# Kernel optimization log

Measured on AMD Instinct MI355X. Metric: run time of the kernel, lower is better.

Reference implementation:

```python
import jax, jax.numpy as jnp
import numpy as np

V = 12000; WE = 1000; FEAT = 2048; FE = 1024; H = 1024; AH = 512; NREG = 36; B = 128; T = 17
PAD_ID = 0


def _lstm_cell(x, h, c, wih, whh, bih, bhh):
    # torch LSTMCell: gates ordered (input, forget, cell, output)
    g = x @ wih.T + h @ whh.T + bih + bhh
    i, f, gg, o = jnp.split(g, 4, axis=-1)
    c_new = jax.nn.sigmoid(f) * c + jax.nn.sigmoid(i) * jnp.tanh(gg)
    h_new = jax.nn.sigmoid(o) * jnp.tanh(c_new)
    return h_new, c_new


def setup_inputs() -> dict:
    key = jax.random.key(0)
    ks = jax.random.split(key, 24)
    s = 0.02
    emb_w = jax.random.normal(ks[0], (V, WE), jnp.float32) * s
    emb_w = emb_w.at[PAD_ID].set(0.0)  # padding_idx row is zero
    inp = {
        'fc_feats': jax.random.normal(ks[1], (B, FEAT), jnp.float32),
        'att_feats': jax.random.normal(ks[2], (B, NREG, FEAT), jnp.float32),
        'captions': jax.random.randint(ks[3], (B, T), 0, V, jnp.int64),
        'emb_w': emb_w,
        'fc_w': jax.random.normal(ks[4], (FEAT, FE), jnp.float32) * s,
        'fc_b': jnp.zeros((FE,), jnp.float32),
        'atte_w': jax.random.normal(ks[5], (FEAT, FE), jnp.float32) * s,
        'atte_b': jnp.zeros((FE,), jnp.float32),
        'ctx_w': jax.random.normal(ks[6], (FE, AH), jnp.float32) * s,
        'ctx_b': jnp.zeros((AH,), jnp.float32),
        'attl_wih': jax.random.normal(ks[7], (4 * H, H + FE + WE), jnp.float32) * s,
        'attl_whh': jax.random.normal(ks[8], (4 * H, H), jnp.float32) * s,
        'attl_bih': jnp.zeros((4 * H,), jnp.float32),
        'attl_bhh': jnp.zeros((4 * H,), jnp.float32),
        'h2att_w': jax.random.normal(ks[9], (H, AH), jnp.float32) * s,
        'h2att_b': jnp.zeros((AH,), jnp.float32),
        'alpha_w': jax.random.normal(ks[10], (AH,), jnp.float32) * s,
        'alpha_b': jnp.zeros((), jnp.float32),
        'langl_wih': jax.random.normal(ks[11], (4 * H, FE + H), jnp.float32) * s,
        'langl_whh': jax.random.normal(ks[12], (4 * H, H), jnp.float32) * s,
        'langl_bih': jnp.zeros((4 * H,), jnp.float32),
        'langl_bhh': jnp.zeros((4 * H,), jnp.float32),
        'cls_w': jax.random.normal(ks[13], (H, V), jnp.float32) * s,
        'cls_b': jnp.zeros((V,), jnp.float32),
    }
    return inp


def _forward(fc_feats, att_feats, captions, emb_w, fc_w, fc_b, atte_w, atte_b,
             ctx_w, ctx_b, attl_wih, attl_whh, attl_bih, attl_bhh,
             h2att_w, h2att_b, alpha_w, alpha_b,
             langl_wih, langl_whh, langl_bih, langl_bhh, cls_w, cls_b):
    # _prepare_features (eval mode: dropout is identity)
    fc_e = jax.nn.relu(fc_feats @ fc_w + fc_b)                 # [B, FE]
    att_e = jax.nn.relu(att_feats @ atte_w + atte_b)           # [B, N, FE]
    p_att = att_e @ ctx_w + ctx_b                              # [B, N, AH]
    bsz = fc_feats.shape[0]
    h0 = jnp.zeros((bsz, H), fc_feats.dtype)

    def step(carry, it):
        h_att, c_att, h_lang, c_lang = carry
        w = jax.nn.relu(emb_w[it])                             # [B, WE]
        x_att = jnp.concatenate([h_lang, fc_e, w], axis=1)
        h_att, c_att = _lstm_cell(x_att, h_att, c_att, attl_wih, attl_whh, attl_bih, attl_bhh)
        # Attention
        hq = h_att @ h2att_w + h2att_b                          # [B, AH]
        e = jnp.tanh(p_att + hq[:, None, :]) @ alpha_w + alpha_b  # [B, N]
        alpha = jax.nn.softmax(e, axis=1)
        att_res = jnp.einsum('bn,bnd->bd', alpha, att_e)        # [B, FE]
        x_lang = jnp.concatenate([att_res, h_att], axis=1)
        h_lang, c_lang = _lstm_cell(x_lang, h_lang, c_lang, langl_wih, langl_whh, langl_bih, langl_bhh)
        logprobs = jax.nn.log_softmax(h_lang @ cls_w + cls_b, axis=1)  # [B, V]
        return (h_att, c_att, h_lang, c_lang), logprobs

    its = captions[:, :-1].T  # [T-1, B]
    _, outs = jax.lax.scan(step, (h0, h0, h0, h0), its)
    return jnp.transpose(outs, (1, 0, 2))  # [B, T-1, V]


def reference(fc_feats, att_feats, captions, emb_w, fc_w, fc_b, atte_w, atte_b,
              ctx_w, ctx_b, attl_wih, attl_whh, attl_bih, attl_bhh,
              h2att_w, h2att_b, alpha_w, alpha_b,
              langl_wih, langl_whh, langl_bih, langl_bhh, cls_w, cls_b):
    return _forward(fc_feats, att_feats, captions, emb_w, fc_w, fc_b, atte_w, atte_b,
                    ctx_w, ctx_b, attl_wih, attl_whh, attl_bih, attl_bhh,
                    h2att_w, h2att_b, alpha_w, alpha_b,
                    langl_wih, langl_whh, langl_bih, langl_bhh, cls_w, cls_b)
```

## Files before the change

kernel.cpp:

```cpp
#include <hip/hip_runtime.h>
#include <cstddef>
#include <cstdint>

constexpr int CV    = 12000;
constexpr int CVP2  = 12288;
constexpr int CWE   = 1000;
constexpr int CFEAT = 2048;
constexpr int CFE   = 1024;
constexpr int CH    = 1024;
constexpr int CAH   = 512;
constexpr int CNREG = 36;
constexpr int CB    = 128;
constexpr int CT    = 17;
constexpr int G4    = 4096;
constexpr int XH    = 2048;
constexpr int XL3   = 3072;

#define CDIV(a,b) (((a)+(b)-1)/(b))

typedef __bf16 bf16_t;
typedef __bf16 bf16x8 __attribute__((ext_vector_type(8)));
typedef __bf16 bf16x4 __attribute__((ext_vector_type(4)));
typedef float  f32x4  __attribute__((ext_vector_type(4)));

typedef __attribute__((address_space(3))) uint32_t lds_u32;
typedef const __attribute__((address_space(1))) uint32_t glb_u32;

struct Seg { const bf16_t* A; const bf16_t* W; int lda, ldw, kt; };

template<bool RELU, bool OUTBF, int SWZ>
__global__ __launch_bounds__(256)
void pre_gemm(Seg s0, int inner, const float* __restrict__ bias1,
              void* __restrict__ Cout, int ldc)
{
    const int tid = threadIdx.x;
    const int wid = tid >> 6, lane = tid & 63;
    const int wr = wid >> 1, wc = wid & 1;
    const int llo = lane & 15, lhi = lane >> 4;
    const int nb = gridDim.x, id = blockIdx.x;
    const int sw = (id & 7) * (nb >> 3) + (id >> 3);
    int m0, n0;
    if (SWZ == 1)      { n0 = (sw / inner) * 64;  m0 = (sw % inner) * 128; }
    else if (SWZ == 2) { m0 = (sw / inner) * 128; n0 = (sw % inner) * 64;  }
    else {
        const int xcd = id & 7, idx = id >> 3;
        m0 = (((xcd >> 2) << 3) + (idx & 7)) * 128;
        n0 = (((xcd & 3) << 4) + (idx >> 3)) * 64;
    }

    __shared__ __align__(16) uint8_t sm[2][24576];

    const int TT = s0.kt;
    f32x4 acc[4][2] = {};
    uint4 ra[4], rb[2];
    const int srow = tid >> 3, sc = tid & 7;
    const int cswz = (sc ^ (srow & 7)) << 4;

    auto load_tile = [&](int ti) {
        const int k0 = ti << 6;
        #pragma unroll
        for (int i = 0; i < 4; ++i)
            ra[i] = *(const uint4*)(s0.A + (size_t)(m0 + i * 32 + srow) * s0.lda + k0 + sc * 8);
        #pragma unroll
        for (int i = 0; i < 2; ++i)
            rb[i] = *(const uint4*)(s0.W + (size_t)(n0 + i * 32 + srow) * s0.ldw + k0 + sc * 8);
    };
    auto write_tile = [&](int buf) {
        uint8_t* base = sm[buf];
        #pragma unroll
        for (int i = 0; i < 4; ++i) *(uint4*)(base + (i * 32 + srow) * 128 + cswz) = ra[i];
        #pragma unroll
        for (int i = 0; i < 2; ++i) *(uint4*)(base + 16384 + (i * 32 + srow) * 128 + cswz) = rb[i];
    };
    auto compute = [&](int buf) {
        const uint8_t* base = sm[buf];
        const int r7 = llo & 7;
        #pragma unroll
        for (int kk = 0; kk < 2; ++kk) {
            const int coff = ((kk * 4 + lhi) ^ r7) << 4;
            bf16x8 af[4], bg[2];
            #pragma unroll
            for (int fm = 0; fm < 4; ++fm)
                af[fm] = *(const bf16x8*)(base + (wr * 64 + fm * 16 + llo) * 128 + coff);
            #pragma unroll
            for (int fn = 0; fn < 2; ++fn)
                bg[fn] = *(const bf16x8*)(base + 16384 + (wc * 32 + fn * 16 + llo) * 128 + coff);
            #pragma unroll
            for (int fm = 0; fm < 4; ++fm)
                #pragma unroll
                for (int fn = 0; fn < 2; ++fn)
                    acc[fm][fn] = __builtin_amdgcn_mfma_f32_16x16x32_bf16(
                        af[fm], bg[fn], acc[fm][fn], 0, 0, 0);
        }
    };

    load_tile(0); write_tile(0);
    load_tile(1);
    __syncthreads();
    int cur = 0;
    for (int ti = 0; ti < TT; ++ti) {
        if (ti + 1 < TT) write_tile(cur ^ 1);
        if (ti + 2 < TT) load_tile(ti + 2);
        compute(cur);
        __syncthreads();
        cur ^= 1;
    }

    if (OUTBF) {
        bf16_t* st = (bf16_t*)sm[0];
        #pragma unroll
        for (int fn = 0; fn < 2; ++fn) {
            const int lcol = wc * 32 + fn * 16 + llo;
            const float b = bias1 ? bias1[n0 + lcol] : 0.f;
            #pragma unroll
            for (int fm = 0; fm < 4; ++fm)
                #pragma unroll
                for (int r = 0; r < 4; ++r) {
                    float v = acc[fm][fn][r] + b;
                    if (RELU) v = fmaxf(v, 0.f);
                    st[(wr * 64 + fm * 16 + lhi * 4 + r) * 64 + lcol] = (bf16_t)v;
                }
        }
        __syncthreads();
        #pragma unroll
        for (int i = 0; i < 4; ++i) {
            const int q = tid + i * 256;
            const int row = q >> 3, ch = q & 7;
            *(uint4*)((bf16_t*)Cout + (size_t)(m0 + row) * ldc + n0 + ch * 8)
                = *(const uint4*)&st[row * 64 + ch * 8];
        }
    } else {
        const int colb = n0 + wc * 32;
        const int rowb = m0 + wr * 64 + lhi * 4;
        #pragma unroll
        for (int fn = 0; fn < 2; ++fn) {
            const int col = colb + fn * 16 + llo;
            const float b = bias1 ? bias1[col] : 0.f;
            #pragma unroll
            for (int fm = 0; fm < 4; ++fm)
                #pragma unroll
                for (int r = 0; r < 4; ++r) {
                    float v = acc[fm][fn][r] + b;
                    if (RELU) v = fmaxf(v, 0.f);
                    ((float*)Cout)[(size_t)(rowb + fm * 16 + r) * ldc + col] = v;
                }
        }
    }
}

__global__ __launch_bounds__(256)
void cls_gemm(const bf16_t* __restrict__ A, const bf16_t* __restrict__ W,
              const float* __restrict__ bias, bf16_t* __restrict__ Cout)
{
    const int tid = threadIdx.x;
    const int wid = tid >> 6, lane = tid & 63;
    const int wr = wid >> 1, wc = wid & 1;
    const int llo = lane & 15, lhi = lane >> 4;
    const int id = blockIdx.x;
    const int xcd = id & 7, idx = id >> 3;
    const int mg = xcd & 1, ng = xcd >> 1;
    const int m0 = (mg * 8 + (idx & 7)) * 128;
    const int n0 = (ng * 24 + (idx >> 3)) * 128;

    __shared__ __align__(16) uint8_t pool[65536];
    auto bufA = [&](int b) { return pool + b * 16384; };
    auto bufB = [&](int b) { return pool + 32768 + b * 16384; };

    constexpr int TT = 16;
    f32x4 acc[4][4] = {};
    uint4 ra[4], rbv[4];

    auto load_tile = [&](int ti) {
        const int k0 = ti << 6;
        #pragma unroll
        for (int i = 0; i < 4; ++i) {
            const int q = tid + i * 256;
            const int row = q >> 3, c = q & 7;
            ra[i]  = *(const uint4*)(A + (size_t)(m0 + row) * CH + k0 + c * 8);
            rbv[i] = *(const uint4*)(W + (size_t)(n0 + row) * CH + k0 + c * 8);
        }
    };
    auto write_tile = [&](int buf) {
        #pragma unroll
        for (int i = 0; i < 4; ++i) {
            const int q = tid + i * 256;
            const int row = q >> 3, c = q & 7;
            const int o = row * 128 + ((c ^ (row & 7)) << 4);
            *(uint4*)(bufA(buf) + o) = ra[i];
            *(uint4*)(bufB(buf) + o) = rbv[i];
        }
    };
    auto compute = [&](int buf) {
        const int r7 = llo & 7;
        #pragma unroll
        for (int kk = 0; kk < 2; ++kk) {
            const int coff = ((kk * 4 + lhi) ^ r7) << 4;
            bf16x8 af[4], bg[4];
            #pragma unroll
            for (int fm = 0; fm < 4; ++fm)
                af[fm] = *(const bf16x8*)(bufA(buf) + (wr * 64 + fm * 16 + llo) * 128 + coff);
            #pragma unroll
            for (int fn = 0; fn < 4; ++fn)
                bg[fn] = *(const bf16x8*)(bufB(buf) + (wc * 64 + fn * 16 + llo) * 128 + coff);
            #pragma unroll
            for (int fm = 0; fm < 4; ++fm)
                #pragma unroll
                for (int fn = 0; fn < 4; ++fn)
                    acc[fm][fn] = __builtin_amdgcn_mfma_f32_16x16x32_bf16(
                        af[fm], bg[fn], acc[fm][fn], 0, 0, 0);
        }
    };

    load_tile(0); write_tile(0);
    load_tile(1);
    __syncthreads();
    int cur = 0;
    for (int ti = 0; ti < TT; ++ti) {
        if (ti + 1 < TT) write_tile(cur ^ 1);
        if (ti + 2 < TT) load_tile(ti + 2);
        compute(cur);
        __syncthreads();
        cur ^= 1;
    }

    constexpr int STR = 136;
    bf16_t* st = (bf16_t*)pool;
    #pragma unroll
    for (int fn = 0; fn < 4; ++fn) {
        const int lcol = wc * 64 + fn * 16 + llo;
        const int col = n0 + lcol;
        const float b = (col < CV) ? bias[col] : 0.f;
        #pragma unroll
        for (int fm = 0; fm < 4; ++fm)
            #pragma unroll
            for (int r = 0; r < 4; ++r)
                st[(wr * 64 + fm * 16 + lhi * 4 + r) * STR + lcol]
                    = (bf16_t)(acc[fm][fn][r] + b);
    }
    __syncthreads();
    #pragma unroll
    for (int i = 0; i < 8; ++i) {
        const int q = tid + i * 256;
        const int row = q >> 4, ch = q & 15;
        *(uint4*)(Cout + (size_t)(m0 + row) * CVP2 + n0 + ch * 8)
            = *(const uint4*)&st[row * STR + ch * 8];
    }
}

template<int TAG>
__global__ __launch_bounds__(256)
void gate_split(const bf16_t* __restrict__ A, int lda,
                const bf16_t* __restrict__ W, int ldw, int ktz,
                bf16_t* __restrict__ gpart)
{
    const int tid = threadIdx.x;
    const int w = tid >> 6, lane = tid & 63;
    const int llo = lane & 15, lhi = lane >> 4;
    const int n0 = blockIdx.x * 16;
    const int z  = blockIdx.y;
    const int kb = z * ktz;

    __shared__ __align__(16) uint8_t sm[4][2][6144];

    f32x4 acc0 = {0.f,0.f,0.f,0.f}, acc1 = {0.f,0.f,0.f,0.f};

    auto stage = [&](int buf, int ti) {
        const int k0 = (kb + ti) << 6;
        uint8_t* base = sm[w][buf];
        #pragma unroll
        for (int i = 0; i < 4; ++i) {
            const int q = lane + i * 64;
            const int row = q >> 3, c = q & 7;
            const int scz = c ^ (row & 7);
            const bf16_t* gp = A + (size_t)(w * 32 + row) * lda + k0 + scz * 8;
            __builtin_amdgcn_global_load_lds((glb_u32*)gp,
                (lds_u32*)(base + i * 1024 + lane * 16), 16, 0, 0);
        }
        #pragma unroll
        for (int i = 0; i < 2; ++i) {
            const int q = lane + i * 64;
            const int row = q >> 3, c = q & 7;
            const int scz = c ^ (row & 7);
            const bf16_t* gp = W + (size_t)(n0 + row) * ldw + k0 + scz * 8;
            __builtin_amdgcn_global_load_lds((glb_u32*)gp,
                (lds_u32*)(base + 4096 + i * 1024 + lane * 16), 16, 0, 0);
        }
    };
    auto compute = [&](int buf) {
        const uint8_t* base = sm[w][buf];
        const int r7 = llo & 7;
        #pragma unroll
        for (int kk = 0; kk < 2; ++kk) {
            const int coff = ((kk * 4 + lhi) ^ r7) << 4;
            bf16x8 a0 = *(const bf16x8*)(base + llo * 128 + coff);
            bf16x8 a1 = *(const bf16x8*)(base + (16 + llo) * 128 + coff);
            bf16x8 bb = *(const bf16x8*)(base + 4096 + llo * 128 + coff);
            acc0 = __builtin_amdgcn_mfma_f32_16x16x32_bf16(a0, bb, acc0, 0, 0, 0);
            acc1 = __builtin_amdgcn_mfma_f32_16x16x32_bf16(a1, bb, acc1, 0, 0, 0);
        }
    };

    stage(0, 0);
    if (ktz > 1) stage(1, 1);
    int cur = 0;
    for (int ti = 0; ti < ktz; ++ti) {
        if (ti + 1 < ktz) asm volatile("s_waitcnt vmcnt(6)" ::: "memory");
        else              asm volatile("s_waitcnt vmcnt(0)" ::: "memory");
        __builtin_amdgcn_sched_barrier(0);
        compute(cur);
        __builtin_amdgcn_sched_barrier(0);
        if (ti + 2 < ktz) stage(cur, ti + 2);
        cur ^= 1;
    }

    bf16_t* gp = gpart + (size_t)z * CB * G4;
    const int col = n0 + llo;
    #pragma unroll
    for (int r = 0; r < 4; ++r) {
        gp[(size_t)(w * 32 + lhi * 4 + r) * G4 + col] = (bf16_t)acc0[r];
        gp[(size_t)(w * 32 + 16 + lhi * 4 + r) * G4 + col] = (bf16_t)acc1[r];
    }
}

__global__ __launch_bounds__(1024)
void lstm_attn(const bf16_t* __restrict__ gpart, const bf16_t* __restrict__ gpre_fc,
               const bf16_t* __restrict__ gemb,
               const float* __restrict__ cbias, float* __restrict__ c_att,
               const bf16_t* __restrict__ p_att, const bf16_t* __restrict__ att_e,
               const bf16_t* __restrict__ h2att_wT, const float* __restrict__ h2att_b,
               const float* __restrict__ alpha_w, const float* __restrict__ alpha_b,
               bf16_t* __restrict__ xh_nxt, bf16_t* __restrict__ xl_cur)
{
    __shared__ float sh[CH];
    __shared__ float shq[CAH];
    __shared__ float se[64], salpha[64];
    const int b = blockIdx.x, tid = threadIdx.x;

    {
        const int j = tid;
        float g0 = 0.f, g1 = 0.f, g2 = 0.f, g3 = 0.f;
        #pragma unroll
        for (int z = 0; z < 4; ++z) {
            bf16x4 g = *(const bf16x4*)(gpart + (size_t)z * CB * G4 + (size_t)b * G4 + 4 * j);
            g0 += (float)g[0]; g1 += (float)g[1]; g2 += (float)g[2]; g3 += (float)g[3];
        }
        f32x4 cb = *(const f32x4*)(cbias + 4 * j);
        bf16x4 gf4 = *(const bf16x4*)(gpre_fc + (size_t)b * G4 + 4 * j);
        bf16x4 ge4 = *(const bf16x4*)(gemb + (size_t)b * G4 + 4 * j);
        const float gi = g0 + cb[0] + (float)gf4[0] + (float)ge4[0];
        const float gf = g1 + cb[1] + (float)gf4[1] + (float)ge4[1];
        const float gg = g2 + cb[2] + (float)gf4[2] + (float)ge4[2];
        const float go = g3 + cb[3] + (float)gf4[3] + (float)ge4[3];
        const float si = 1.f / (1.f + expf(-gi));
        const float sf = 1.f / (1.f + expf(-gf));
        const float so = 1.f / (1.f + expf(-go));
        const float cn = sf * c_att[b * CH + j] + si * tanhf(gg);
        const float hn = so * tanhf(cn);
        c_att[b * CH + j] = cn;
        sh[j] = hn;
        const bf16_t hb = (bf16_t)hn;
        xh_nxt[(size_t)b * XH + 1024 + j] = hb;
        xl_cur[(size_t)b * XL3 + 1024 + j] = hb;
    }
    __syncthreads();

    {
        const int q2 = tid & 1, n = tid >> 1;
        const bf16_t* wrow = h2att_wT + (size_t)n * CH + q2 * 512;
        float s = 0.f;
        #pragma unroll 4
        for (int k = 0; k < 512; k += 8) {
            bf16x8 w8 = *(const bf16x8*)(wrow + k);
            #pragma unroll
            for (int j = 0; j < 8; ++j) s = fmaf((float)w8[j], sh[q2 * 512 + k + j], s);
        }
        s += __shfl_xor(s, 1);
        if (q2 == 0) shq[n] = s + h2att_b[n];
    }
    __syncthreads();

    {
        const int wave = tid >> 6, lane = tid & 63;
        for (int n = wave; n < CNREG; n += 16) {
            const bf16_t* pr = p_att + ((size_t)b * CNREG + n) * CAH;
            float s = 0.f;
            #pragma unroll
            for (int q = 0; q < CAH / 64; ++q) {
                const int d = lane + q * 64;
                s += alpha_w[d] * tanhf((float)pr[d] + shq[d]);
            }
            for (int off = 32; off; off >>= 1) s += __shfl_down(s, off);
            if (lane == 0) se[n] = s + alpha_b[0];
        }
    }
    __syncthreads();

    {
        float mx = -1e30f;
        for (int n = 0; n < CNREG; ++n) mx = fmaxf(mx, se[n]);
        float sum = 0.f;
        for (int n = 0; n < CNREG; ++n) sum += expf(se[n] - mx);
        if (tid < CNREG) salpha[tid] = expf(se[tid] - mx) / sum;
    }
    __syncthreads();

    {
        const int d = tid;
        float s = 0.f;
        const bf16_t* ae = att_e + (size_t)b * CNREG * CFE + d;
        #pragma unroll 4
        for (int n = 0; n < CNREG; ++n)
            s = fmaf(salpha[n], (float)ae[(size_t)n * CFE], s);
        xl_cur[(size_t)b * XL3 + d] = (bf16_t)s;
    }
}

__global__ __launch_bounds__(256)
void lstm_flat(const bf16_t* __restrict__ gpart, const float* __restrict__ cbias,
               float* __restrict__ c,
               bf16_t* __restrict__ xh_nxt, bf16_t* __restrict__ xl_nxt,
               bf16_t* __restrict__ h_all, int t)
{
    const int idx = blockIdx.x * 256 + threadIdx.x;
    const int b = idx >> 10, j = idx & 1023;
    float g0 = 0.f, g1 = 0.f, g2 = 0.f, g3 = 0.f;
    #pragma unroll
    for (int z = 0; z < 4; ++z) {
        bf16x4 g = *(const bf16x4*)(gpart + (size_t)z * CB * G4 + (size_t)b * G4 + 4 * j);
        g0 += (float)g[0]; g1 += (float)g[1]; g2 += (float)g[2]; g3 += (float)g[3];
    }
    f32x4 cb = *(const f32x4*)(cbias + 4 * j);
    const float si = 1.f / (1.f + expf(-(g0 + cb[0])));
    const float sf = 1.f / (1.f + expf(-(g1 + cb[1])));
    const float so = 1.f / (1.f + expf(-(g3 + cb[3])));
    const float cn = sf * c[idx] + si * tanhf(g2 + cb[2]);
    const float hn = so * tanhf(cn);
    c[idx] = cn;
    const bf16_t hb = (bf16_t)hn;
    xh_nxt[(size_t)b * XH + j] = hb;
    xl_nxt[(size_t)b * XL3 + 2048 + j] = hb;
    h_all[((size_t)b * (CT - 1) + t) * CH + j] = hb;
}

__global__ void convert_pad(const float* __restrict__ src, bf16_t* __restrict__ dst,
                            int C, int Cp)
{
    const int r = blockIdx.y;
    const int c = blockIdx.x * 256 + threadIdx.x;
    if (c >= Cp) return;
    dst[(size_t)r * Cp + c] = (c < C) ? (bf16_t)src[(size_t)r * C + c] : (bf16_t)0.f;
}

__global__ void convert_perm(const float* __restrict__ src, int srcld, int scol0,
                             int valid, bf16_t* __restrict__ dst, int dstld, int dcol0,
                             int ncols)
{
    const int rp = blockIdx.y;
    const int c = blockIdx.x * 256 + threadIdx.x;
    if (c >= ncols) return;
    const int rs = (rp & 3) * 1024 + (rp >> 2);
    const float v = (c < valid) ? src[(size_t)rs * srcld + scol0 + c] : 0.f;
    dst[(size_t)rp * dstld + dcol0 + c] = (bf16_t)v;
}

__global__ void bias_perm(const float* __restrict__ bih, const float* __restrict__ bhh,
                          float* __restrict__ dst)
{
    const int rp = blockIdx.x * 256 + threadIdx.x;
    if (rp >= G4) return;
    const int rs = (rp & 3) * 1024 + (rp >> 2);
    dst[rp] = bih[rs] + bhh[rs];
}

__global__ __launch_bounds__(256)
void transpose_convert(const float* __restrict__ src, bf16_t* __restrict__ dst,
                       int K, int N)
{
    __shared__ float tile[32][33];
    const int n0 = blockIdx.x * 32, k0 = blockIdx.y * 32;
    const int tx = threadIdx.x & 31, ty = threadIdx.x >> 5;
    #pragma unroll
    for (int i = 0; i < 4; ++i) {
        const int k = k0 + ty + i * 8, n = n0 + tx;
        tile[ty + i * 8][tx] = (k < K && n < N) ? src[(size_t)k * N + n] : 0.f;
    }
    __syncthreads();
    #pragma unroll
    for (int i = 0; i < 4; ++i) {
        const int n = n0 + ty + i * 8, k = k0 + tx;
        if (n < N && k < K) dst[(size_t)n * K + k] = (bf16_t)tile[tx][ty + i * 8];
    }
}

__global__ void emb_all(const float* __restrict__ emb_w,
                        const int* __restrict__ captions, bf16_t* __restrict__ w_emb)
{
    const int r = blockIdx.y;
    const int j = blockIdx.x * 256 + threadIdx.x;
    const int t = r >> 7, b = r & 127;
    const int tok = captions[b * CT + t];
    const float v = (j < CWE) ? fmaxf(emb_w[(size_t)tok * CWE + j], 0.f) : 0.f;
    w_emb[(size_t)r * 1024 + j] = (bf16_t)v;
}

__global__ __launch_bounds__(256)
void logsoftmax_bf(const bf16_t* __restrict__ lg, float* __restrict__ out)
{
    __shared__ float red[4];
    const int r = blockIdx.x, tid = threadIdx.x;
    const bf16_t* row = lg + (size_t)r * CVP2;

    float v[48];
    float mx = -1e30f;
    #pragma unroll
    for (int i = 0; i < 6; ++i) {
        const int c = tid + i * 256;
        if (c < 1500) {
            bf16x8 x = *(const bf16x8*)(row + c * 8);
            #pragma unroll
            for (int j = 0; j < 8; ++j) {
                v[i * 8 + j] = (float)x[j];
                mx = fmaxf(mx, v[i * 8 + j]);
            }
        } else {
            #pragma unroll
            for (int j = 0; j < 8; ++j) v[i * 8 + j] = -1e30f;
        }
    }
    for (int off = 32; off; off >>= 1) mx = fmaxf(mx, __shfl_down(mx, off));
    if ((tid & 63) == 0) red[tid >> 6] = mx;
    __syncthreads();
    mx = fmaxf(fmaxf(red[0], red[1]), fmaxf(red[2], red[3]));
    __syncthreads();

    float sum = 0.f;
    #pragma unroll
    for (int i = 0; i < 6; ++i)
        if (tid + i * 256 < 1500)
            #pragma unroll
            for (int j = 0; j < 8; ++j) sum += expf(v[i * 8 + j] - mx);
    for (int off = 32; off; off >>= 1) sum += __shfl_down(sum, off);
    if ((tid & 63) == 0) red[tid >> 6] = sum;
    __syncthreads();
    sum = red[0] + red[1] + red[2] + red[3];
    const float lse = mx + logf(sum);

    #pragma unroll
    for (int i = 0; i < 6; ++i) {
        const int c = tid + i * 256;
        if (c < 1500) {
            float* o = out + (size_t)r * CV + c * 8;
            float4 a = make_float4(v[i*8+0]-lse, v[i*8+1]-lse, v[i*8+2]-lse, v[i*8+3]-lse);
            float4 bq = make_float4(v[i*8+4]-lse, v[i*8+5]-lse, v[i*8+6]-lse, v[i*8+7]-lse);
            *(float4*)o = a;
            *(float4*)(o + 4) = bq;
        }
    }
}

extern "C" void kernel_launch(void* const* d_in, const int* in_sizes, int n_in,
                              void* d_out, int out_size, void* d_ws, size_t ws_size,
                              hipStream_t stream)
{
    const float* fc_feats  = (const float*)d_in[0];
    const float* att_feats = (const float*)d_in[1];
    const int*   captions  = (const int*)  d_in[2];
    const float* emb_w     = (const float*)d_in[3];
    const float* fc_w      = (const float*)d_in[4];
    const float* fc_b      = (const float*)d_in[5];
    const float* atte_w    = (const float*)d_in[6];
    const float* atte_b    = (const float*)d_in[7];
    const float* ctx_w     = (const float*)d_in[8];
    const float* ctx_b     = (const float*)d_in[9];
    const float* attl_wih  = (const float*)d_in[10];
    const float* attl_whh  = (const float*)d_in[11];
    const float* attl_bih  = (const float*)d_in[12];
    const float* attl_bhh  = (const float*)d_in[13];
    const float* h2att_w   = (const float*)d_in[14];
    const float* h2att_b   = (const float*)d_in[15];
    const float* alpha_w   = (const float*)d_in[16];
    const float* alpha_b   = (const float*)d_in[17];
    const float* langl_wih = (const float*)d_in[18];
    const float* langl_whh = (const float*)d_in[19];
    const float* langl_bih = (const float*)d_in[20];
    const float* langl_bhh = (const float*)d_in[21];
    const float* cls_w     = (const float*)d_in[22];
    const float* cls_b     = (const float*)d_in[23];

    float* out = (float*)d_out;

    char* p = (char*)d_ws;
    auto alloc_bf = [&](size_t e) { bf16_t* q = (bf16_t*)p; p += e * 2; return q; };
    auto alloc_f  = [&](size_t e) { float*  q = (float*) p; p += e * 4; return q; };

    bf16_t* Wcat_att    = alloc_bf((size_t)G4 * XH);
    bf16_t* Wcat_lang   = alloc_bf((size_t)G4 * XL3);
    bf16_t* Win_fc      = alloc_bf((size_t)G4 * 1024);
    bf16_t* Win_emb     = alloc_bf((size_t)G4 * 1024);
    bf16_t* fc_wT_b     = alloc_bf((size_t)CFE * CFEAT);
    bf16_t* atte_wT_b   = alloc_bf((size_t)CFE * CFEAT);
    bf16_t* ctx_wT_b    = alloc_bf((size_t)CAH * CFE);
    bf16_t* h2att_wT_b  = alloc_bf((size_t)CAH * CH);
    bf16_t* cls_wT_b    = alloc_bf((size_t)CVP2 * CH);
    bf16_t* fc_feats_b  = alloc_bf((size_t)CB * CFEAT);
    bf16_t* att_feats_b = alloc_bf((size_t)CB * CNREG * CFEAT);
    bf16_t* att_e_b     = alloc_bf((size_t)CB * CNREG * CFE);
    bf16_t* w_emb       = alloc_bf((size_t)(CT - 1) * CB * 1024);
    bf16_t* fc_e_b      = alloc_bf((size_t)CB * CFE);
    bf16_t* gpre_fc     = alloc_bf((size_t)CB * G4);
    bf16_t* xh0         = alloc_bf((size_t)CB * XH);
    bf16_t* xh1         = alloc_bf((size_t)CB * XH);
    bf16_t* xl3a        = alloc_bf((size_t)CB * XL3);
    bf16_t* xl3b        = alloc_bf((size_t)CB * XL3);
    bf16_t* h_all       = alloc_bf((size_t)CB * (CT - 1) * CH);
    bf16_t* p_att       = alloc_bf((size_t)CB * CNREG * CAH);
    bf16_t* gpart       = alloc_bf((size_t)4 * CB * G4);
    float*  cbias_att   = alloc_f (G4);
    float*  cbias_lang  = alloc_f (G4);
    float*  c_att       = alloc_f ((size_t)CB * CH);
    float*  c_lang      = alloc_f ((size_t)CB * CH);

    bf16_t* Gemb   = att_feats_b;
    bf16_t* logits = Wcat_att;

    hipMemsetAsync(xh0,    0, (size_t)CB * XH * 2, stream);
    hipMemsetAsync(xh1,    0, (size_t)CB * XH * 2, stream);
    hipMemsetAsync(xl3a,   0, (size_t)CB * XL3 * 2, stream);
    hipMemsetAsync(xl3b,   0, (size_t)CB * XL3 * 2, stream);
    hipMemsetAsync(c_att,  0, (size_t)CB * CH * 4, stream);
    hipMemsetAsync(c_lang, 0, (size_t)CB * CH * 4, stream);
    hipMemsetAsync(cls_wT_b + (size_t)CV * CH, 0, (size_t)(CVP2 - CV) * CH * 2, stream);

    const dim3 blk(256);
    auto mk = [](const bf16_t* A, int lda, const bf16_t* W, int ldw, int kt) {
        return Seg{A, W, lda, ldw, kt};
    };

    convert_perm<<<dim3(4, G4), blk, 0, stream>>>(attl_wih, 3048, 0, 1024, Wcat_att, XH, 0, 1024);
    convert_perm<<<dim3(4, G4), blk, 0, stream>>>(attl_whh, 1024, 0, 1024, Wcat_att, XH, 1024, 1024);
    convert_perm<<<dim3(4, G4), blk, 0, stream>>>(attl_wih, 3048, 1024, 1024, Win_fc, 1024, 0, 1024);
    convert_perm<<<dim3(4, G4), blk, 0, stream>>>(attl_wih, 3048, 2048, 1000, Win_emb, 1024, 0, 1024);
    convert_perm<<<dim3(8, G4), blk, 0, stream>>>(langl_wih, 2048, 0, 2048, Wcat_lang, XL3, 0, 2048);
    convert_perm<<<dim3(4, G4), blk, 0, stream>>>(langl_whh, 1024, 0, 1024, Wcat_lang, XL3, 2048, 1024);
    bias_perm<<<16, blk, 0, stream>>>(attl_bih, attl_bhh, cbias_att);
    bias_perm<<<16, blk, 0, stream>>>(langl_bih, langl_bhh, cbias_lang);
    convert_pad<<<dim3(8, CB), blk, 0, stream>>>(fc_feats, fc_feats_b, CFEAT, CFEAT);
    convert_pad<<<dim3(8, CB * CNREG), blk, 0, stream>>>(att_feats, att_feats_b, CFEAT, CFEAT);
    transpose_convert<<<dim3(CFE/32, CFEAT/32), blk, 0, stream>>>(fc_w,    fc_wT_b,    CFEAT, CFE);
    transpose_convert<<<dim3(CFE/32, CFEAT/32), blk, 0, stream>>>(atte_w,  atte_wT_b,  CFEAT, CFE);
    transpose_convert<<<dim3(CAH/32, CFE/32),   blk, 0, stream>>>(ctx_w,   ctx_wT_b,   CFE,   CAH);
    transpose_convert<<<dim3(CAH/32, CH/32),    blk, 0, stream>>>(h2att_w, h2att_wT_b, CH,    CAH);
    transpose_convert<<<dim3(CDIV(CV,32), CH/32), blk, 0, stream>>>(cls_w, cls_wT_b,   CH,    CV);
    emb_all<<<dim3(4, (CT - 1) * CB), blk, 0, stream>>>(emb_w, captions, w_emb);

    pre_gemm<true,true,2><<<16, blk, 0, stream>>>(
        mk(fc_feats_b, CFEAT, fc_wT_b, CFEAT, 32), 16, fc_b, fc_e_b, CFE);
    pre_gemm<true,true,2><<<576, blk, 0, stream>>>(
        mk(att_feats_b, CFEAT, atte_wT_b, CFEAT, 32), 16, atte_b, att_e_b, CFE);
    pre_gemm<false,true,2><<<288, blk, 0, stream>>>(
        mk(att_e_b, CFE, ctx_wT_b, CFE, 16), 8, ctx_b, p_att, CAH);
    pre_gemm<false,true,1><<<64, blk, 0, stream>>>(
        mk(fc_e_b, CFE, Win_fc, 1024, 16), 1, nullptr, gpre_fc, G4);
    pre_gemm<false,true,3><<<1024, blk, 0, stream>>>(
        mk(w_emb, 1024, Win_emb, 1024, 16), 0, nullptr, Gemb, G4);

    for (int t = 0; t < CT - 1; ++t) {
        bf16_t* xh_cur = (t & 1) ? xh1 : xh0;
        bf16_t* xh_nxt = (t & 1) ? xh0 : xh1;
        bf16_t* xl_cur = (t & 1) ? xl3b : xl3a;
        bf16_t* xl_nxt = (t & 1) ? xl3a : xl3b;

        gate_split<0><<<dim3(256, 4), blk, 0, stream>>>(
            xh_cur, XH, Wcat_att, XH, 8, gpart);

        lstm_attn<<<CB, dim3(1024), 0, stream>>>(
            gpart, gpre_fc, Gemb + (size_t)t * CB * G4, cbias_att, c_att,
            p_att, att_e_b, h2att_wT_b, h2att_b, alpha_w, alpha_b,
            xh_nxt, xl_cur);

        gate_split<1><<<dim3(256, 4), blk, 0, stream>>>(
            xl_cur, XL3, Wcat_lang, XL3, 12, gpart);

        lstm_flat<<<512, blk, 0, stream>>>(
            gpart, cbias_lang, c_lang, xh_nxt, xl_nxt, h_all, t);
    }

    cls_gemm<<<1536, blk, 0, stream>>>(h_all, cls_wT_b, cls_b, logits);
    logsoftmax_bf<<<2048, blk, 0, stream>>>(logits, out);
}
```

Before: 1.918 ms.

## Fuse gate GEMMs with LSTM/attention tails using last-arriving-block atomic counters

Merges each per-step gate GEMM with its following LSTM-cell (and attention) kernel. Every block counts its arrival on a global atomic counter, and the last 128 blocks to arrive spin until all 1024 have finished, then each handles one batch row. This cuts the per-step launches from four to two and removes the launch gaps between them. In exchange the tail work for each row now runs in a 256-thread block instead of 1024, with loops restructured to suit, and correctness relies on all blocks making forward progress and on the fences.

```diff
diff --git a/kernel.cpp b/kernel.cpp
--- a/kernel.cpp
+++ b/kernel.cpp
@@ -15,6 +15,8 @@
 constexpr int G4    = 4096;
 constexpr int XH    = 2048;
 constexpr int XL3   = 3072;
+constexpr int NGB   = 1024;
+constexpr int NTAIL = 128;
 
 #define CDIV(a,b) (((a)+(b)-1)/(b))
 
@@ -247,20 +249,14 @@
     }
 }
 
-template<int TAG>
-__global__ __launch_bounds__(256)
-void gate_split(const bf16_t* __restrict__ A, int lda,
-                const bf16_t* __restrict__ W, int ldw, int ktz,
-                bf16_t* __restrict__ gpart)
+__device__ __forceinline__ void gate_core(
+    const bf16_t* __restrict__ A, int lda,
+    const bf16_t* __restrict__ W, int ldw, int ktz, int kb, int n0,
+    uint8_t (*sm)[2][6144], bf16_t* __restrict__ gp)
 {
     const int tid = threadIdx.x;
     const int w = tid >> 6, lane = tid & 63;
     const int llo = lane & 15, lhi = lane >> 4;
-    const int n0 = blockIdx.x * 16;
-    const int z  = blockIdx.y;
-    const int kb = z * ktz;
-
-    __shared__ __align__(16) uint8_t sm[4][2][6144];
 
     f32x4 acc0 = {0.f,0.f,0.f,0.f}, acc1 = {0.f,0.f,0.f,0.f};
 
@@ -272,8 +268,8 @@
             const int q = lane + i * 64;
             const int row = q >> 3, c = q & 7;
             const int scz = c ^ (row & 7);
-            const bf16_t* gp = A + (size_t)(w * 32 + row) * lda + k0 + scz * 8;
-            __builtin_amdgcn_global_load_lds((glb_u32*)gp,
+            const bf16_t* gpt = A + (size_t)(w * 32 + row) * lda + k0 + scz * 8;
+            __builtin_amdgcn_global_load_lds((glb_u32*)gpt,
                 (lds_u32*)(base + i * 1024 + lane * 16), 16, 0, 0);
         }
         #pragma unroll
@@ -281,8 +277,8 @@
             const int q = lane + i * 64;
             const int row = q >> 3, c = q & 7;
             const int scz = c ^ (row & 7);
-            const bf16_t* gp = W + (size_t)(n0 + row) * ldw + k0 + scz * 8;
-            __builtin_amdgcn_global_load_lds((glb_u32*)gp,
+            const bf16_t* gpt = W + (size_t)(n0 + row) * ldw + k0 + scz * 8;
+            __builtin_amdgcn_global_load_lds((glb_u32*)gpt,
                 (lds_u32*)(base + 4096 + i * 1024 + lane * 16), 16, 0, 0);
         }
     };
@@ -313,7 +309,6 @@
         cur ^= 1;
     }
 
-    bf16_t* gp = gpart + (size_t)z * CB * G4;
     const int col = n0 + llo;
     #pragma unroll
     for (int r = 0; r < 4; ++r) {
@@ -322,26 +317,61 @@
     }
 }
 
-__global__ __launch_bounds__(1024)
-void lstm_attn(const bf16_t* __restrict__ gpart, const bf16_t* __restrict__ gpre_fc,
-               const bf16_t* __restrict__ gemb,
-               const float* __restrict__ cbias, float* __restrict__ c_att,
-               const bf16_t* __restrict__ p_att, const bf16_t* __restrict__ att_e,
-               const bf16_t* __restrict__ h2att_wT, const float* __restrict__ h2att_b,
-               const float* __restrict__ alpha_w, const float* __restrict__ alpha_b,
-               bf16_t* __restrict__ xh_nxt, bf16_t* __restrict__ xl_cur)
-{
-    __shared__ float sh[CH];
-    __shared__ float shq[CAH];
-    __shared__ float se[64], salpha[64];
-    const int b = blockIdx.x, tid = threadIdx.x;
-
-    {
-        const int j = tid;
+__device__ __forceinline__ int arrive(int* cnt, int* srank)
+{
+    __syncthreads();
+    if (threadIdx.x == 0) {
+        __threadfence();
+        *srank = atomicAdd(cnt, 1);
+    }
+    __syncthreads();
+    return *srank;
+}
+
+__device__ __forceinline__ void spin_until(int* cnt, int target)
+{
+    if (threadIdx.x == 0) {
+        while (*(volatile int*)cnt < target) __builtin_amdgcn_s_sleep(8);
+    }
+    __syncthreads();
+    __threadfence();
+}
+
+__global__ __launch_bounds__(256)
+void gate_att_fused(const bf16_t* __restrict__ A, const bf16_t* __restrict__ W,
+                    bf16_t* __restrict__ gpart, int* __restrict__ cnt,
+                    const bf16_t* __restrict__ gpre_fc, const bf16_t* __restrict__ gemb,
+                    const float* __restrict__ cbias, float* __restrict__ c_att,
+                    const bf16_t* __restrict__ p_att, const bf16_t* __restrict__ att_e,
+                    const bf16_t* __restrict__ h2att_wT, const float* __restrict__ h2att_b,
+                    const float* __restrict__ alpha_w, const float* __restrict__ alpha_b,
+                    bf16_t* __restrict__ xh_nxt, bf16_t* __restrict__ xl_cur)
+{
+    __shared__ __align__(16) uint8_t sm[4][2][6144];
+    __shared__ int srank;
+
+    const int n0 = blockIdx.x * 16;
+    const int z  = blockIdx.y;
+    gate_core(A, XH, W, XH, 8, z * 8, n0, sm, gpart + (size_t)z * CB * G4);
+
+    const int rank = arrive(cnt, &srank);
+    if (rank < NGB - NTAIL) return;
+    spin_until(cnt, NGB);
+    const int b = rank - (NGB - NTAIL);
+    const int tid = threadIdx.x;
+
+    float* sh  = (float*)sm;
+    float* shq = sh + CH;
+    float* se  = shq + CAH;
+    float* sal = se + 64;
+
+    #pragma unroll
+    for (int k4 = 0; k4 < 4; ++k4) {
+        const int j = tid + k4 * 256;
         float g0 = 0.f, g1 = 0.f, g2 = 0.f, g3 = 0.f;
         #pragma unroll
-        for (int z = 0; z < 4; ++z) {
-            bf16x4 g = *(const bf16x4*)(gpart + (size_t)z * CB * G4 + (size_t)b * G4 + 4 * j);
+        for (int zz = 0; zz < 4; ++zz) {
+            bf16x4 g = *(const bf16x4*)(gpart + (size_t)zz * CB * G4 + (size_t)b * G4 + 4 * j);
             g0 += (float)g[0]; g1 += (float)g[1]; g2 += (float)g[2]; g3 += (float)g[3];
         }
         f32x4 cb = *(const f32x4*)(cbias + 4 * j);
@@ -365,23 +395,26 @@
     __syncthreads();
 
     {
-        const int q2 = tid & 1, n = tid >> 1;
-        const bf16_t* wrow = h2att_wT + (size_t)n * CH + q2 * 512;
-        float s = 0.f;
-        #pragma unroll 4
-        for (int k = 0; k < 512; k += 8) {
-            bf16x8 w8 = *(const bf16x8*)(wrow + k);
-            #pragma unroll
-            for (int j = 0; j < 8; ++j) s = fmaf((float)w8[j], sh[q2 * 512 + k + j], s);
-        }
-        s += __shfl_xor(s, 1);
-        if (q2 == 0) shq[n] = s + h2att_b[n];
+        const int q4 = tid & 3;
+        for (int n = tid >> 2; n < CAH; n += 64) {
+            const bf16_t* wrow = h2att_wT + (size_t)n * CH + q4 * 256;
+            float s = 0.f;
+            #pragma unroll 4
+            for (int k = 0; k < 256; k += 8) {
+                bf16x8 w8 = *(const bf16x8*)(wrow + k);
+                #pragma unroll
+                for (int j = 0; j < 8; ++j) s = fmaf((float)w8[j], sh[q4 * 256 + k + j], s);
+            }
+            s += __shfl_xor(s, 1);
+            s += __shfl_xor(s, 2);
+            if (q4 == 0) shq[n] = s + h2att_b[n];
+        }
     }
     __syncthreads();
 
     {
         const int wave = tid >> 6, lane = tid & 63;
-        for (int n = wave; n < CNREG; n += 16) {
+        for (int n = wave; n < CNREG; n += 4) {
             const bf16_t* pr = p_att + ((size_t)b * CNREG + n) * CAH;
             float s = 0.f;
             #pragma unroll
@@ -400,46 +433,69 @@
         for (int n = 0; n < CNREG; ++n) mx = fmaxf(mx, se[n]);
         float sum = 0.f;
         for (int n = 0; n < CNREG; ++n) sum += expf(se[n] - mx);
-        if (tid < CNREG) salpha[tid] = expf(se[tid] - mx) / sum;
+        if (tid < CNREG) sal[tid] = expf(se[tid] - mx) / sum;
     }
     __syncthreads();
 
     {
-        const int d = tid;
-        float s = 0.f;
-        const bf16_t* ae = att_e + (size_t)b * CNREG * CFE + d;
+        const int d0 = tid * 4;
+        float a0 = 0.f, a1 = 0.f, a2 = 0.f, a3 = 0.f;
+        const bf16_t* ae = att_e + (size_t)b * CNREG * CFE + d0;
         #pragma unroll 4
-        for (int n = 0; n < CNREG; ++n)
-            s = fmaf(salpha[n], (float)ae[(size_t)n * CFE], s);
-        xl_cur[(size_t)b * XL3 + d] = (bf16_t)s;
+        for (int n = 0; n < CNREG; ++n) {
+            bf16x4 v = *(const bf16x4*)(ae + (size_t)n * CFE);
+            const float al = sal[n];
+            a0 = fmaf(al, (float)v[0], a0);
+            a1 = fmaf(al, (float)v[1], a1);
+            a2 = fmaf(al, (float)v[2], a2);
+            a3 = fmaf(al, (float)v[3], a3);
+        }
+        bf16x4 o = { (bf16_t)a0, (bf16_t)a1, (bf16_t)a2, (bf16_t)a3 };
+        *(bf16x4*)(xl_cur + (size_t)b * XL3 + d0) = o;
     }
 }
 
 __global__ __launch_bounds__(256)
-void lstm_flat(const bf16_t* __restrict__ gpart, const float* __restrict__ cbias,
-               float* __restrict__ c,
-               bf16_t* __restrict__ xh_nxt, bf16_t* __restrict__ xl_nxt,
-               bf16_t* __restrict__ h_all, int t)
-{
-    const int idx = blockIdx.x * 256 + threadIdx.x;
-    const int b = idx >> 10, j = idx & 1023;
-    float g0 = 0.f, g1 = 0.f, g2 = 0.f, g3 = 0.f;
-    #pragma unroll
-    for (int z = 0; z < 4; ++z) {
-        bf16x4 g = *(const bf16x4*)(gpart + (size_t)z * CB * G4 + (size_t)b * G4 + 4 * j);
-        g0 += (float)g[0]; g1 += (float)g[1]; g2 += (float)g[2]; g3 += (float)g[3];
-    }
-    f32x4 cb = *(const f32x4*)(cbias + 4 * j);
-    const float si = 1.f / (1.f + expf(-(g0 + cb[0])));
-    const float sf = 1.f / (1.f + expf(-(g1 + cb[1])));
-    const float so = 1.f / (1.f + expf(-(g3 + cb[3])));
-    const float cn = sf * c[idx] + si * tanhf(g2 + cb[2]);
-    const float hn = so * tanhf(cn);
-    c[idx] = cn;
-    const bf16_t hb = (bf16_t)hn;
-    xh_nxt[(size_t)b * XH + j] = hb;
-    xl_nxt[(size_t)b * XL3 + 2048 + j] = hb;
-    h_all[((size_t)b * (CT - 1) + t) * CH + j] = hb;
+void gate_lang_fused(const bf16_t* __restrict__ A, const bf16_t* __restrict__ W,
+                     bf16_t* __restrict__ gpart, int* __restrict__ cnt,
+                     const float* __restrict__ cbias, float* __restrict__ c,
+                     bf16_t* __restrict__ xh_nxt, bf16_t* __restrict__ xl_nxt,
+                     bf16_t* __restrict__ h_all, int t)
+{
+    __shared__ __align__(16) uint8_t sm[4][2][6144];
+    __shared__ int srank;
+
+    const int n0 = blockIdx.x * 16;
+    const int z  = blockIdx.y;
+    gate_core(A, XL3, W, XL3, 12, z * 12, n0, sm, gpart + (size_t)z * CB * G4);
+
+    const int rank = arrive(cnt, &srank);
+    if (rank < NGB - NTAIL) return;
+    spin_until(cnt, NGB);
+    const int b = rank - (NGB - NTAIL);
+    const int tid = threadIdx.x;
+
+    #pragma unroll
+    for (int k4 = 0; k4 < 4; ++k4) {
+        const int j = tid + k4 * 256;
+        float g0 = 0.f, g1 = 0.f, g2 = 0.f, g3 = 0.f;
+        #pragma unroll
+        for (int zz = 0; zz < 4; ++zz) {
+            bf16x4 g = *(const bf16x4*)(gpart + (size_t)zz * CB * G4 + (size_t)b * G4 + 4 * j);
+            g0 += (float)g[0]; g1 += (float)g[1]; g2 += (float)g[2]; g3 += (float)g[3];
+        }
+        f32x4 cb = *(const f32x4*)(cbias + 4 * j);
+        const float si = 1.f / (1.f + expf(-(g0 + cb[0])));
+        const float sf = 1.f / (1.f + expf(-(g1 + cb[1])));
+        const float so = 1.f / (1.f + expf(-(g3 + cb[3])));
+        const float cn = sf * c[b * CH + j] + si * tanhf(g2 + cb[2]);
+        const float hn = so * tanhf(cn);
+        c[b * CH + j] = cn;
+        const bf16_t hb = (bf16_t)hn;
+        xh_nxt[(size_t)b * XH + j] = hb;
+        xl_nxt[(size_t)b * XL3 + 2048 + j] = hb;
+        h_all[((size_t)b * (CT - 1) + t) * CH + j] = hb;
+    }
 }
 
 __global__ void convert_pad(const float* __restrict__ src, bf16_t* __restrict__ dst,
@@ -619,6 +675,7 @@
     float*  cbias_lang  = alloc_f (G4);
     float*  c_att       = alloc_f ((size_t)CB * CH);
     float*  c_lang      = alloc_f ((size_t)CB * CH);
+    int*    counters    = (int*)p; p += 64 * sizeof(int);
 
     bf16_t* Gemb   = att_feats_b;
     bf16_t* logits = Wcat_att;
@@ -630,6 +687,7 @@
     hipMemsetAsync(c_att,  0, (size_t)CB * CH * 4, stream);
     hipMemsetAsync(c_lang, 0, (size_t)CB * CH * 4, stream);
     hipMemsetAsync(cls_wT_b + (size_t)CV * CH, 0, (size_t)(CVP2 - CV) * CH * 2, stream);
+    hipMemsetAsync(counters, 0, 64 * sizeof(int), stream);
 
     const dim3 blk(256);
     auto mk = [](const bf16_t* A, int lda, const bf16_t* W, int ldw, int kt) {
@@ -670,19 +728,15 @@
         bf16_t* xl_cur = (t & 1) ? xl3b : xl3a;
         bf16_t* xl_nxt = (t & 1) ? xl3a : xl3b;
 
-        gate_split<0><<<dim3(256, 4), blk, 0, stream>>>(
-            xh_cur, XH, Wcat_att, XH, 8, gpart);
-
-        lstm_attn<<<CB, dim3(1024), 0, stream>>>(
-            gpart, gpre_fc, Gemb + (size_t)t * CB * G4, cbias_att, c_att,
+        gate_att_fused<<<dim3(256, 4), blk, 0, stream>>>(
+            xh_cur, Wcat_att, gpart, counters + t * 2,
+            gpre_fc, Gemb + (size_t)t * CB * G4, cbias_att, c_att,
             p_att, att_e_b, h2att_wT_b, h2att_b, alpha_w, alpha_b,
             xh_nxt, xl_cur);
 
-        gate_split<1><<<dim3(256, 4), blk, 0, stream>>>(
-            xl_cur, XL3, Wcat_lang, XL3, 12, gpart);
-
-        lstm_flat<<<512, blk, 0, stream>>>(
-            gpart, cbias_lang, c_lang, xh_nxt, xl_nxt, h_all, t);
+        gate_lang_fused<<<dim3(256, 4), blk, 0, stream>>>(
+            xl_cur, Wcat_lang, gpart, counters + t * 2 + 1,
+            cbias_lang, c_lang, xh_nxt, xl_nxt, h_all, t);
     }
 
     cls_gemm<<<1536, blk, 0, stream>>>(h_all, cls_wT_b, cls_b, logits);
```

New measurement: 4.340 ms. 2.26x slower.
